# Kernel tuning notes

Measured on AMD Instinct MI355X. Metric: run time of the kernel, lower is better.

The kernel has to match this reference:

```python
import jax, jax.numpy as jnp
import numpy as np

H = 256          # hidden_size
HH, WW = 4, 4
CONV = HH * WW * H   # 4096, conv_out_size
N = 16           # n_subtasks
S = 32           # subtask_size
B = 256          # batch
T = 128          # timesteps
TOT = N + S + H + S + 1 + 1  # 338, RecurrentState width


def setup_inputs() -> dict:
    key = jax.random.key(0)
    ks = jax.random.split(key, 12)
    w = lambda k, shape: (jax.random.normal(k, shape) * 0.02).astype(jnp.float32)
    obs = jax.random.normal(ks[0], (T, B, CONV), jnp.float32)
    task = jax.random.normal(ks[1], (B, N, S), jnp.float32)
    hx0 = jnp.zeros((B, TOT), jnp.float32).at[:, :N].set(1.0 / N)  # uniform pointer init
    return dict(
        obs=obs, task=task, hx0=hx0,
        W_ih=w(ks[2], (3 * H, H)), W_hh=w(ks[3], (3 * H, H)),
        b_ih=jnp.zeros((3 * H,), jnp.float32), b_hh=jnp.zeros((3 * H,), jnp.float32),
        W_f=w(ks[4], (H, CONV + 2 * S + 1)), b_f=jnp.zeros((H,), jnp.float32),
        W_u=w(ks[5], (1, 2 * H)), b_u=jnp.zeros((1,), jnp.float32),
        W_s=w(ks[6], (3, H)), b_s=jnp.zeros((3,), jnp.float32),
        W_pi=w(ks[7], (N, H + S)), b_pi=jnp.zeros((N,), jnp.float32),
        W_beta=w(ks[8], (2, CONV + S)), b_beta=jnp.zeros((2,), jnp.float32),
    )


def reference(obs, task, hx0, W_ih, W_hh, b_ih, b_hh, W_f, b_f, W_u, b_u,
              W_s, b_s, W_pi, b_pi, W_beta, b_beta):
    M = task  # [B, N, S] subtask memory
    p0 = hx0[:, :N]
    r0 = hx0[:, N:N + S]
    h0 = hx0[:, N + S:N + S + H]
    g0 = hx0[:, N + S + H:N + S + H + S]
    b0 = hx0[:, N + S + H + S:N + S + H + S + 1]
    keys = jax.random.split(jax.random.key(42), T * 2).reshape(T, 2)

    def gru(x, h):  # torch.nn.GRUCell math
        gi = x @ W_ih.T + b_ih
        gh = h @ W_hh.T + b_hh
        ir, iz, inn = jnp.split(gi, 3, axis=-1)
        hr, hz, hn = jnp.split(gh, 3, axis=-1)
        rr = jax.nn.sigmoid(ir + hr)
        z = jax.nn.sigmoid(iz + hz)
        n = jnp.tanh(inn + rr * hn)
        return (1.0 - z) * n + z * h

    def step(carry, xs):
        p, r, h, b = carry[0], carry[1], carry[2], carry[4]
        g = carry[3]
        x, kk = xs
        # s = f(cat(x, r, g, b))
        s = jnp.concatenate([x, r, g, b], axis=-1) @ W_f.T + b_f
        # update gate c = sigmoid(phi_update(cat(s, h)))
        c = jax.nn.sigmoid(jnp.concatenate([s, h], axis=-1) @ W_u.T + b_u)  # [B,1]
        h_new = gru(s, h)
        # pointer shift: l = softmax(phi_shift(h_old)); p = conv1d(p, l) (same-pad, k=3)
        l = jax.nn.softmax(h @ W_s.T + b_s, axis=1)  # [B,3]
        pp = jnp.pad(p, ((0, 0), (1, 1)))
        p_new = l[:, 0:1] * pp[:, :N] + l[:, 1:2] * pp[:, 1:N + 1] + l[:, 2:3] * pp[:, 2:N + 2]
        # memory read r = p @ M
        r_new = jnp.einsum('bn,bns->bs', p_new, M)
        p = c * p_new + (1.0 - c) * p
        r = c * r_new + (1.0 - c) * r
        h = c * h_new + (1.0 - c) * h
        # sample g ~ Cat(pi_theta(h, r)); g embedding = selected memory row
        logits_g = jnp.concatenate([h, r], axis=-1) @ W_pi.T + b_pi  # [B,N]
        g_idx = jax.random.categorical(kk[0], logits_g)  # [B] int
        lp_g = jnp.take_along_axis(jax.nn.log_softmax(logits_g, axis=-1), g_idx[:, None], axis=1)  # [B,1]
        g_vec = jnp.take_along_axis(M, g_idx[:, None, None], axis=1)[:, 0, :]  # [B,S]
        g = c * g_vec + (1.0 - c) * g
        # sample b ~ Cat(beta(x, g))
        logits_b = jnp.concatenate([x, g], axis=-1) @ W_beta.T + b_beta  # [B,2]
        b_idx = jax.random.categorical(kk[1], logits_b)
        lp_b = jnp.take_along_axis(jax.nn.log_softmax(logits_b, axis=-1), b_idx[:, None], axis=1)
        b = b_idx[:, None].astype(jnp.float32)
        log_prob = lp_g + lp_b
        out = jnp.concatenate([p, r, h, g, b, log_prob], axis=-1)  # [B, TOT]
        return (p, r, h, g, b), out

    _, outs = jax.lax.scan(step, (p0, r0, h0, g0, b0), (obs, keys))
    return outs  # [T, B, TOT]
```

## Files before the change

### kernel.cpp

```cpp
#include <hip/hip_runtime.h>


#define RNG_PARTITIONABLE 1

#define T_STEPS 128
#define B_ROWS  256
#define TOT     338
#define CONV    4096
#define LDWF    4161
#define LDWB    4128

__device__ __forceinline__ void tf2x32(unsigned k0, unsigned k1, unsigned c0, unsigned c1,
                                       unsigned &o0, unsigned &o1) {
  const unsigned ks2 = k0 ^ k1 ^ 0x1BD11BDAu;
  unsigned x0 = c0 + k0;
  unsigned x1 = c1 + k1;
#define TFR(r) { x0 += x1; x1 = (x1 << (r)) | (x1 >> (32 - (r))); x1 ^= x0; }
  TFR(13) TFR(15) TFR(26) TFR(6)
  x0 += k1; x1 += ks2 + 1u;
  TFR(17) TFR(29) TFR(16) TFR(24)
  x0 += ks2; x1 += k0 + 2u;
  TFR(13) TFR(15) TFR(26) TFR(6)
  x0 += k0; x1 += k1 + 3u;
  TFR(17) TFR(29) TFR(16) TFR(24)
  x0 += k1; x1 += ks2 + 4u;
  TFR(13) TFR(15) TFR(26) TFR(6)
  x0 += ks2; x1 += k0 + 5u;
#undef TFR
  o0 = x0; o1 = x1;
}

__device__ __forceinline__ void rng_key(unsigned j, unsigned &k0, unsigned &k1) {
#if RNG_PARTITIONABLE
  tf2x32(0u, 42u, 0u, j, k0, k1);
#else
  unsigned w[2];
  for (int q = 0; q < 2; ++q) {
    unsigned i = 2u*j + (unsigned)q, a, b;
    if (i < 256u) { tf2x32(0u, 42u, i, 256u + i, a, b); w[q] = a; }
    else          { tf2x32(0u, 42u, i - 256u, i, a, b); w[q] = b; }
  }
  k0 = w[0]; k1 = w[1];
#endif
}

__device__ __forceinline__ unsigned rng_bits(unsigned k0, unsigned k1, unsigned idx, unsigned total) {
#if RNG_PARTITIONABLE
  unsigned o0, o1;
  tf2x32(k0, k1, 0u, idx, o0, o1);
  return o0 ^ o1;
#else
  unsigned half = total >> 1, o0, o1;
  if (idx < half) { tf2x32(k0, k1, idx, half + idx, o0, o1); return o0; }
  else            { tf2x32(k0, k1, idx - half, idx, o0, o1); return o1; }
#endif
}

__device__ __forceinline__ float gumbel_from_bits(unsigned bits) {
  float u0 = __uint_as_float(0x3f800000u | (bits >> 9)) - 1.0f;
  float u  = fmaxf(u0, 1.17549435e-38f);
  return -logf(-logf(u));
}

__global__ __launch_bounds__(256) void rng_k(float* __restrict__ ggum, float* __restrict__ bgum) {
  unsigned tid = blockIdx.x * 256u + threadIdx.x;
  const unsigned NG = T_STEPS * B_ROWS * 16;
  const unsigned NB = T_STEPS * B_ROWS * 2;
  if (tid < NG) {
    unsigned t = tid / (B_ROWS * 16);
    unsigned i = tid % (B_ROWS * 16);
    unsigned k0, k1; rng_key(2u * t, k0, k1);
    ggum[tid] = gumbel_from_bits(rng_bits(k0, k1, i, B_ROWS * 16));
  } else if (tid < NG + NB) {
    unsigned q = tid - NG;
    unsigned t = q / (B_ROWS * 2);
    unsigned i = q % (B_ROWS * 2);
    unsigned k0, k1; rng_key(2u * t + 1u, k0, k1);
    bgum[q] = gumbel_from_bits(rng_bits(k0, k1, i, B_ROWS * 2));
  }
}

__global__ __launch_bounds__(256) void prep2_k(const float* __restrict__ W_ih,
                                               const float* __restrict__ W_hh,
                                               float2* __restrict__ WT2) {
  int col = blockIdx.x;
  int k = threadIdx.x;
  WT2[(size_t)k * 768 + col] =
      make_float2(W_ih[(size_t)col * 256 + k], W_hh[(size_t)col * 256 + k]);
}

__device__ __forceinline__ float waveRed(float v) {
  v += __shfl_down(v, 32, 64);
  v += __shfl_down(v, 16, 64);
  v += __shfl_down(v, 8, 64);
  v += __shfl_down(v, 4, 64);
  v += __shfl_down(v, 2, 64);
  v += __shfl_down(v, 1, 64);
  return v;
}

__global__ __launch_bounds__(256) void bx_k(const float* __restrict__ obs,
                                            const float* __restrict__ W_beta,
                                            const float* __restrict__ b_beta,
                                            float* __restrict__ bxv) {
  int m = blockIdx.x, tid = threadIdx.x;
  const float* row = obs + (size_t)m * CONV;
  float p0 = 0.f, p1 = 0.f;
  for (int i = tid; i < CONV; i += 256) {
    float o = row[i];
    p0 = fmaf(o, W_beta[i], p0);
    p1 = fmaf(o, W_beta[LDWB + i], p1);
  }
  p0 = waveRed(p0); p1 = waveRed(p1);
  __shared__ float sc[2][4];
  int w = tid >> 6;
  if ((tid & 63) == 0) { sc[0][w] = p0; sc[1][w] = p1; }
  __syncthreads();
  if (tid == 0) bxv[(size_t)m * 2 + 0] = sc[0][0] + sc[0][1] + sc[0][2] + sc[0][3] + b_beta[0];
  if (tid == 1) bxv[(size_t)m * 2 + 1] = sc[1][0] + sc[1][1] + sc[1][2] + sc[1][3] + b_beta[1];
}

struct __attribute__((packed, aligned(4))) F4 { float x, y, z, w; };

__global__ __launch_bounds__(256) void gemm1_k(const float* __restrict__ A,
                                               const float* __restrict__ W,
                                               const float* __restrict__ bias,
                                               float* __restrict__ C1) {
  __shared__ __align__(16) float As[32][68];
  __shared__ __align__(16) float Bs[32][68];
  int bid = blockIdx.x;
  int mt = bid & 511, nt = bid >> 9;
  int m0 = mt * 64, n0 = nt * 64;
  int tid = threadIdx.x;
  int tm = tid & 15, tn = tid >> 4;
  int lr = tid >> 2;
  int lc = (tid & 3) * 8;
  float acc[4][4] = {};
  for (int k0 = 0; k0 < CONV; k0 += 32) {
    F4 a0 = *(const F4*)(A + (size_t)(m0 + lr) * CONV + k0 + lc);
    F4 a1 = *(const F4*)(A + (size_t)(m0 + lr) * CONV + k0 + lc + 4);
    F4 b0 = *(const F4*)(W + (size_t)(n0 + lr) * LDWF + k0 + lc);
    F4 b1 = *(const F4*)(W + (size_t)(n0 + lr) * LDWF + k0 + lc + 4);
    __syncthreads();
    As[lc + 0][lr] = a0.x; As[lc + 1][lr] = a0.y; As[lc + 2][lr] = a0.z; As[lc + 3][lr] = a0.w;
    As[lc + 4][lr] = a1.x; As[lc + 5][lr] = a1.y; As[lc + 6][lr] = a1.z; As[lc + 7][lr] = a1.w;
    Bs[lc + 0][lr] = b0.x; Bs[lc + 1][lr] = b0.y; Bs[lc + 2][lr] = b0.z; Bs[lc + 3][lr] = b0.w;
    Bs[lc + 4][lr] = b1.x; Bs[lc + 5][lr] = b1.y; Bs[lc + 6][lr] = b1.z; Bs[lc + 7][lr] = b1.w;
    __syncthreads();
#pragma unroll
    for (int kk = 0; kk < 32; ++kk) {
      const float4 av = *(const float4*)&As[kk][tm * 4];
      const float4 bv = *(const float4*)&Bs[kk][tn * 4];
      acc[0][0] = fmaf(av.x, bv.x, acc[0][0]); acc[0][1] = fmaf(av.x, bv.y, acc[0][1]);
      acc[0][2] = fmaf(av.x, bv.z, acc[0][2]); acc[0][3] = fmaf(av.x, bv.w, acc[0][3]);
      acc[1][0] = fmaf(av.y, bv.x, acc[1][0]); acc[1][1] = fmaf(av.y, bv.y, acc[1][1]);
      acc[1][2] = fmaf(av.y, bv.z, acc[1][2]); acc[1][3] = fmaf(av.y, bv.w, acc[1][3]);
      acc[2][0] = fmaf(av.z, bv.x, acc[2][0]); acc[2][1] = fmaf(av.z, bv.y, acc[2][1]);
      acc[2][2] = fmaf(av.z, bv.z, acc[2][2]); acc[2][3] = fmaf(av.z, bv.w, acc[2][3]);
      acc[3][0] = fmaf(av.w, bv.x, acc[3][0]); acc[3][1] = fmaf(av.w, bv.y, acc[3][1]);
      acc[3][2] = fmaf(av.w, bv.z, acc[3][2]); acc[3][3] = fmaf(av.w, bv.w, acc[3][3]);
    }
  }
  const int mrow = m0 + tm * 4;
  const int ncol = n0 + tn * 4;
  float4 bv4 = *(const float4*)(bias + ncol);
#pragma unroll
  for (int i = 0; i < 4; ++i) {
    float4 v;
    v.x = acc[i][0] + bv4.x; v.y = acc[i][1] + bv4.y;
    v.z = acc[i][2] + bv4.z; v.w = acc[i][3] + bv4.w;
    *(float4*)(C1 + (size_t)(mrow + i) * 256 + ncol) = v;
  }
}

__global__ __launch_bounds__(768, 1) void seq_k(
    const float* __restrict__ hx0, const float* __restrict__ task,
    const float* __restrict__ W_f, const float* __restrict__ WT2,
    const float* __restrict__ b_ih, const float* __restrict__ b_hh,
    const float* __restrict__ W_u, const float* __restrict__ b_u,
    const float* __restrict__ W_s, const float* __restrict__ b_s,
    const float* __restrict__ W_pi, const float* __restrict__ b_pi,
    const float* __restrict__ W_beta, const float* __restrict__ C1,
    const float* __restrict__ bxv, const float* __restrict__ ggum,
    const float* __restrict__ bgum, float* __restrict__ out) {
  const int b = blockIdx.x;
  const int tid = threadIdx.x;
  const int o = tid & 255;
  const int part = tid >> 8;
  const float2* __restrict__ WT2v = (const float2*)WT2;

  __shared__ float wf_sh[65 * 256];
  __shared__ float wpi_sh[288 * 16];
  __shared__ float2 shb[256];
  __shared__ float2 gsum[2][256];
  __shared__ float M_sh[512];
  __shared__ float p_sh[16], pn_sh[16], r_sh[32], g_sh[32];
  __shared__ float red4[4][4];
  __shared__ float red16[4][16];
  __shared__ float logit_sh[16];
  __shared__ float l_sh[3];
  __shared__ float c_sh, b_sh;
  __shared__ int gidx_sh;
  __shared__ float misc_sh[3];
  __shared__ float gg_sh[16], bg_sh[2], bx_sh[2];
  __shared__ float wb_sh[2][32], bpi_sh[16];

  for (int i = tid; i < 65 * 256; i += 768) {
    int oo = i / 65, j = i % 65;
    wf_sh[i] = W_f[(size_t)oo * LDWF + CONV + j];
  }
  for (int i = tid; i < 288 * 16; i += 768) wpi_sh[i] = W_pi[i];
  if (part == 0) shb[o] = make_float2(0.f, hx0[b * TOT + 48 + o]);
  if (tid < 16) p_sh[tid] = hx0[b * TOT + tid];
  if (tid < 32) {
    r_sh[tid] = hx0[b * TOT + 16 + tid];
    g_sh[tid] = hx0[b * TOT + 304 + tid];
    wb_sh[0][tid] = W_beta[CONV + tid];
    wb_sh[1][tid] = W_beta[LDWB + CONV + tid];
  }
  if (tid >= 32 && tid < 48) bpi_sh[tid - 32] = b_pi[tid - 32];
  if (tid == 0) b_sh = hx0[b * TOT + 336];
  if (tid < 512) M_sh[tid] = task[(size_t)b * 512 + tid];

  const float bih_r = b_ih[o], bih_z = b_ih[256 + o], bih_n = b_ih[512 + o];
  const float bhh_r = b_hh[o], bhh_z = b_hh[256 + o], bhh_n = b_hh[512 + o];
  const float wu_s = W_u[o], wu_h = W_u[256 + o];
  const float ws0 = W_s[o], ws1 = W_s[256 + o], ws2 = W_s[512 + o];
  const float bu0 = b_u[0], bs0 = b_s[0], bs1 = b_s[1], bs2 = b_s[2];
  __syncthreads();

  float c1v = (part == 0) ? C1[(size_t)b * 256 + o] : 0.f;
  float sacc = 0.f, hold = 0.f;

  for (int t = 0; t < T_STEPS; ++t) {
    if (part == 0) {
      hold = shb[o].y;
      sacc = c1v;
      const float* wfr = wf_sh + o * 65;
#pragma unroll
      for (int j = 0; j < 32; ++j) sacc = fmaf(r_sh[j], wfr[j], sacc);
#pragma unroll
      for (int j = 0; j < 32; ++j) sacc = fmaf(g_sh[j], wfr[32 + j], sacc);
      sacc = fmaf(b_sh, wfr[64], sacc);
      shb[o].x = sacc;
    }
    __syncthreads();

    if (part == 0) {
      int tn2 = (t + 1 < T_STEPS) ? t + 1 : t;
      c1v = C1[((size_t)tn2 * 256 + b) * 256 + o];
    } else if (tid < 272) {
      gg_sh[tid - 256] = ggum[((size_t)t * 256 + b) * 16 + (tid - 256)];
    } else if (tid < 274) {
      bg_sh[tid - 272] = bgum[((size_t)t * 256 + b) * 2 + (tid - 272)];
    } else if (tid < 276) {
      bx_sh[tid - 274] = bxv[((size_t)t * 256 + b) * 2 + (tid - 274)];
    }

    float ai = 0.f, ah = 0.f;
#pragma unroll 8
    for (int k = 0; k < 256; ++k) {
      float2 w = WT2v[(size_t)k * 768 + tid];
      float2 sh2 = shb[k];
      ai = fmaf(sh2.x, w.x, ai);
      ah = fmaf(sh2.y, w.y, ah);
    }
    if (part == 0) {
      float pc = fmaf(wu_s, sacc, wu_h * hold);
      float q0 = ws0 * hold, q1 = ws1 * hold, q2 = ws2 * hold;
      pc = waveRed(pc); q0 = waveRed(q0); q1 = waveRed(q1); q2 = waveRed(q2);
      int w4 = tid >> 6;
      if ((tid & 63) == 0) { red4[w4][0] = pc; red4[w4][1] = q0; red4[w4][2] = q1; red4[w4][3] = q2; }
    } else {
      gsum[part - 1][o] = make_float2(ai, ah);
    }
    __syncthreads();
    if (tid == 0) {
      float cs = red4[0][0] + red4[1][0] + red4[2][0] + red4[3][0] + bu0;
      c_sh = 1.0f / (1.0f + expf(-cs));
      float x0 = red4[0][1] + red4[1][1] + red4[2][1] + red4[3][1] + bs0;
      float x1 = red4[0][2] + red4[1][2] + red4[2][2] + red4[3][2] + bs1;
      float x2 = red4[0][3] + red4[1][3] + red4[2][3] + red4[3][3] + bs2;
      float m = fmaxf(x0, fmaxf(x1, x2));
      float e0 = expf(x0 - m), e1 = expf(x1 - m), e2 = expf(x2 - m);
      float es = e0 + e1 + e2;
      l_sh[0] = e0 / es; l_sh[1] = e1 / es; l_sh[2] = e2 / es;
    }
    __syncthreads();
    const float c = c_sh, omc = 1.0f - c;
    float hg = 0.f;
    if (part == 0) {
      float2 gz = gsum[0][o];
      float2 gn = gsum[1][o];
      float rr = 1.0f / (1.0f + expf(-(ai + bih_r + ah + bhh_r)));
      float zz = 1.0f / (1.0f + expf(-(gz.x + bih_z + gz.y + bhh_z)));
      float nn = tanhf(gn.x + bih_n + rr * (gn.y + bhh_n));
      float hnew = (1.0f - zz) * nn + zz * hold;
      hg = c * hnew + omc * hold;
      shb[o].y = hg;
    }
    if (tid < 16) {
      float pm1 = (tid > 0) ? p_sh[tid - 1] : 0.f;
      float pp1 = (tid < 15) ? p_sh[tid + 1] : 0.f;
      pn_sh[tid] = l_sh[0] * pm1 + l_sh[1] * p_sh[tid] + l_sh[2] * pp1;
    }
    __syncthreads();
    float rv = 0.f;
    if (tid < 32) {
      float acc = 0.f;
#pragma unroll
      for (int n2 = 0; n2 < 16; ++n2) acc = fmaf(pn_sh[n2], M_sh[n2 * 32 + tid], acc);
      rv = c * acc + omc * r_sh[tid];
      r_sh[tid] = rv;
    }
    if (tid < 16) p_sh[tid] = c * pn_sh[tid] + omc * p_sh[tid];
    if (part == 0) {
      float pv[16];
#pragma unroll
      for (int o2 = 0; o2 < 16; ++o2) pv[o2] = hg * wpi_sh[o2 * 288 + tid];
      if (tid < 32) {
#pragma unroll
        for (int o2 = 0; o2 < 16; ++o2) pv[o2] = fmaf(rv, wpi_sh[o2 * 288 + 256 + tid], pv[o2]);
      }
#pragma unroll
      for (int o2 = 0; o2 < 16; ++o2) pv[o2] = waveRed(pv[o2]);
      int w4 = tid >> 6;
      if ((tid & 63) == 0) {
#pragma unroll
        for (int o2 = 0; o2 < 16; ++o2) red16[w4][o2] = pv[o2];
      }
    }
    __syncthreads();
    if (tid < 16)
      logit_sh[tid] = red16[0][tid] + red16[1][tid] + red16[2][tid] + red16[3][tid] + bpi_sh[tid];
    __syncthreads();
    if (tid == 0) {
      float best = -3.402823466e+38f; int gidx = 0;
      for (int n2 = 0; n2 < 16; ++n2) {
        float v = logit_sh[n2] + gg_sh[n2];
        if (v > best) { best = v; gidx = n2; }
      }
      float mx = logit_sh[0];
      for (int n2 = 1; n2 < 16; ++n2) mx = fmaxf(mx, logit_sh[n2]);
      float se = 0.f;
      for (int n2 = 0; n2 < 16; ++n2) se += expf(logit_sh[n2] - mx);
      misc_sh[0] = logit_sh[gidx] - mx - logf(se);
      gidx_sh = gidx;
    }
    __syncthreads();
    if (tid < 32) g_sh[tid] = c * M_sh[gidx_sh * 32 + tid] + omc * g_sh[tid];
    __syncthreads();
    if (tid == 0) {
      float lb0 = bx_sh[0], lb1 = bx_sh[1];
      for (int s2 = 0; s2 < 32; ++s2) {
        float gv = g_sh[s2];
        lb0 = fmaf(gv, wb_sh[0][s2], lb0);
        lb1 = fmaf(gv, wb_sh[1][s2], lb1);
      }
      int bidx = ((lb1 + bg_sh[1]) > (lb0 + bg_sh[0])) ? 1 : 0;
      float mb = fmaxf(lb0, lb1);
      float seb = expf(lb0 - mb) + expf(lb1 - mb);
      float lpb = (bidx ? lb1 : lb0) - mb - logf(seb);
      misc_sh[1] = (float)bidx;
      misc_sh[2] = misc_sh[0] + lpb;
      b_sh = (float)bidx;
    }
    __syncthreads();
    if (tid < TOT) {
      size_t base = ((size_t)t * 256 + b) * TOT;
      float v;
      if (tid < 16) v = p_sh[tid];
      else if (tid < 48) v = r_sh[tid - 16];
      else if (tid < 304) v = shb[tid - 48].y;
      else if (tid < 336) v = g_sh[tid - 304];
      else if (tid == 336) v = misc_sh[1];
      else v = misc_sh[2];
      out[base + tid] = v;
    }
    __syncthreads();
  }
}

extern "C" void kernel_launch(void* const* d_in, const int* in_sizes, int n_in,
                              void* d_out, int out_size, void* d_ws, size_t ws_size,
                              hipStream_t stream) {
  const float* obs    = (const float*)d_in[0];
  const float* task   = (const float*)d_in[1];
  const float* hx0    = (const float*)d_in[2];
  const float* W_ih   = (const float*)d_in[3];
  const float* W_hh   = (const float*)d_in[4];
  const float* b_ih   = (const float*)d_in[5];
  const float* b_hh   = (const float*)d_in[6];
  const float* W_f    = (const float*)d_in[7];
  const float* b_f    = (const float*)d_in[8];
  const float* W_u    = (const float*)d_in[9];
  const float* b_u    = (const float*)d_in[10];
  const float* W_s    = (const float*)d_in[11];
  const float* b_s    = (const float*)d_in[12];
  const float* W_pi   = (const float*)d_in[13];
  const float* b_pi   = (const float*)d_in[14];
  const float* W_beta = (const float*)d_in[15];
  const float* b_beta = (const float*)d_in[16];

  char* ws = (char*)d_ws;
  size_t off = 0;
  auto take = [&](size_t bytes) {
    size_t r = off;
    off += (bytes + 255) & ~(size_t)255;
    return r;
  };
  size_t off_WT2  = take((size_t)768 * 256 * 8);
  size_t off_ggum = take((size_t)T_STEPS * B_ROWS * 16 * 4);
  size_t off_bgum = take((size_t)T_STEPS * B_ROWS * 2 * 4);
  size_t off_bx   = take((size_t)T_STEPS * B_ROWS * 2 * 4);
  size_t off_C1   = take((size_t)T_STEPS * B_ROWS * 256 * 4);
  if (off > ws_size) return;

  float* WT2  = (float*)(ws + off_WT2);
  float* ggum = (float*)(ws + off_ggum);
  float* bgum = (float*)(ws + off_bgum);
  float* bxv  = (float*)(ws + off_bx);
  float* C1   = (float*)(ws + off_C1);

  hipLaunchKernelGGL(prep2_k, dim3(768), dim3(256), 0, stream, W_ih, W_hh, (float2*)WT2);
  hipLaunchKernelGGL(rng_k, dim3(2304), dim3(256), 0, stream, ggum, bgum);
  hipLaunchKernelGGL(gemm1_k, dim3(2048), dim3(256), 0, stream, obs, W_f, b_f, C1);
  hipLaunchKernelGGL(bx_k, dim3(32768), dim3(256), 0, stream, obs, W_beta, b_beta, bxv);
  hipLaunchKernelGGL(seq_k, dim3(256), dim3(768), 0, stream,
                     hx0, task, W_f, WT2, b_ih, b_hh, W_u, b_u, W_s, b_s, W_pi, b_pi,
                     W_beta, C1, bxv, ggum, bgum, (float*)d_out);
}
```

Before: 4.590 ms.

## Process four batch rows per sequential block and use packed FMA in GEMM

The sequential recurrent kernel now handles four batch rows per block (64 blocks of 1024 threads instead of 256 of 768). Each load of the W_ih/W_hh weights from global memory is reused across four rows, using packed two-wide FMAs on interleaved hidden-state vectors. This cuts the weight traffic per step roughly fourfold but uses only 64 workgroups, leaving most compute units idle, and adds more per-row shared state. The obs GEMM inner loop is also rewritten with two-wide vector FMAs in the hope of emitting packed FMA instructions.

```diff
diff --git a/kernel.cpp b/kernel.cpp
--- a/kernel.cpp
+++ b/kernel.cpp
@@ -9,6 +9,8 @@
 #define CONV    4096
 #define LDWF    4161
 #define LDWB    4128
+
+typedef float v2f __attribute__((ext_vector_type(2)));
 
 __device__ __forceinline__ void tf2x32(unsigned k0, unsigned k1, unsigned c0, unsigned c1,
                                        unsigned &o0, unsigned &o1) {
@@ -135,7 +137,9 @@
   int tm = tid & 15, tn = tid >> 4;
   int lr = tid >> 2;
   int lc = (tid & 3) * 8;
-  float acc[4][4] = {};
+  v2f acc[4][2];
+#pragma unroll
+  for (int i = 0; i < 4; ++i) { acc[i][0] = (v2f){0.f, 0.f}; acc[i][1] = (v2f){0.f, 0.f}; }
   for (int k0 = 0; k0 < CONV; k0 += 32) {
     F4 a0 = *(const F4*)(A + (size_t)(m0 + lr) * CONV + k0 + lc);
     F4 a1 = *(const F4*)(A + (size_t)(m0 + lr) * CONV + k0 + lc + 4);
@@ -151,14 +155,15 @@
     for (int kk = 0; kk < 32; ++kk) {
       const float4 av = *(const float4*)&As[kk][tm * 4];
       const float4 bv = *(const float4*)&Bs[kk][tn * 4];
-      acc[0][0] = fmaf(av.x, bv.x, acc[0][0]); acc[0][1] = fmaf(av.x, bv.y, acc[0][1]);
-      acc[0][2] = fmaf(av.x, bv.z, acc[0][2]); acc[0][3] = fmaf(av.x, bv.w, acc[0][3]);
-      acc[1][0] = fmaf(av.y, bv.x, acc[1][0]); acc[1][1] = fmaf(av.y, bv.y, acc[1][1]);
-      acc[1][2] = fmaf(av.y, bv.z, acc[1][2]); acc[1][3] = fmaf(av.y, bv.w, acc[1][3]);
-      acc[2][0] = fmaf(av.z, bv.x, acc[2][0]); acc[2][1] = fmaf(av.z, bv.y, acc[2][1]);
-      acc[2][2] = fmaf(av.z, bv.z, acc[2][2]); acc[2][3] = fmaf(av.z, bv.w, acc[2][3]);
-      acc[3][0] = fmaf(av.w, bv.x, acc[3][0]); acc[3][1] = fmaf(av.w, bv.y, acc[3][1]);
-      acc[3][2] = fmaf(av.w, bv.z, acc[3][2]); acc[3][3] = fmaf(av.w, bv.w, acc[3][3]);
+      const v2f bl = (v2f){bv.x, bv.y};
+      const v2f bh = (v2f){bv.z, bv.w};
+      const float aa[4] = {av.x, av.y, av.z, av.w};
+#pragma unroll
+      for (int i = 0; i < 4; ++i) {
+        v2f ax = (v2f){aa[i], aa[i]};
+        acc[i][0] = __builtin_elementwise_fma(ax, bl, acc[i][0]);
+        acc[i][1] = __builtin_elementwise_fma(ax, bh, acc[i][1]);
+      }
     }
   }
   const int mrow = m0 + tm * 4;
@@ -167,13 +172,13 @@
 #pragma unroll
   for (int i = 0; i < 4; ++i) {
     float4 v;
-    v.x = acc[i][0] + bv4.x; v.y = acc[i][1] + bv4.y;
-    v.z = acc[i][2] + bv4.z; v.w = acc[i][3] + bv4.w;
+    v.x = acc[i][0].x + bv4.x; v.y = acc[i][0].y + bv4.y;
+    v.z = acc[i][1].x + bv4.z; v.w = acc[i][1].y + bv4.w;
     *(float4*)(C1 + (size_t)(mrow + i) * 256 + ncol) = v;
   }
 }
 
-__global__ __launch_bounds__(768, 1) void seq_k(
+__global__ __launch_bounds__(1024, 1) void seq_k(
     const float* __restrict__ hx0, const float* __restrict__ task,
     const float* __restrict__ W_f, const float* __restrict__ WT2,
     const float* __restrict__ b_ih, const float* __restrict__ b_hh,
@@ -183,44 +188,51 @@
     const float* __restrict__ W_beta, const float* __restrict__ C1,
     const float* __restrict__ bxv, const float* __restrict__ ggum,
     const float* __restrict__ bgum, float* __restrict__ out) {
-  const int b = blockIdx.x;
+  const int b4 = blockIdx.x;
   const int tid = threadIdx.x;
+  const int r = tid >> 8;
   const int o = tid & 255;
-  const int part = tid >> 8;
+  const int brow = b4 * 4 + r;
   const float2* __restrict__ WT2v = (const float2*)WT2;
 
   __shared__ float wf_sh[65 * 256];
   __shared__ float wpi_sh[288 * 16];
-  __shared__ float2 shb[256];
-  __shared__ float2 gsum[2][256];
-  __shared__ float M_sh[512];
-  __shared__ float p_sh[16], pn_sh[16], r_sh[32], g_sh[32];
-  __shared__ float red4[4][4];
-  __shared__ float red16[4][16];
-  __shared__ float logit_sh[16];
-  __shared__ float l_sh[3];
-  __shared__ float c_sh, b_sh;
-  __shared__ int gidx_sh;
-  __shared__ float misc_sh[3];
-  __shared__ float gg_sh[16], bg_sh[2], bx_sh[2];
+  __shared__ float4 sh01[256];
+  __shared__ float4 sh23[256];
+  __shared__ float gpub[24][256];
+  __shared__ float M_sh[4][512];
+  __shared__ float p_sh[4][16], pn_sh[4][16], r_sh[4][32], g_sh[4][32];
+  __shared__ float red4[4][4][4];
+  __shared__ float red16[4][4][16];
+  __shared__ float logit_sh[4][16];
+  __shared__ float l_sh[4][3];
+  __shared__ float c_sh[4], b_sh[4];
+  __shared__ int gidx_sh[4];
+  __shared__ float misc_sh[4][3];
+  __shared__ float gg_sh[4][16], bg_sh[4][2], bx_sh[4][2];
   __shared__ float wb_sh[2][32], bpi_sh[16];
 
-  for (int i = tid; i < 65 * 256; i += 768) {
+  for (int i = tid; i < 65 * 256; i += 1024) {
     int oo = i / 65, j = i % 65;
     wf_sh[i] = W_f[(size_t)oo * LDWF + CONV + j];
   }
-  for (int i = tid; i < 288 * 16; i += 768) wpi_sh[i] = W_pi[i];
-  if (part == 0) shb[o] = make_float2(0.f, hx0[b * TOT + 48 + o]);
-  if (tid < 16) p_sh[tid] = hx0[b * TOT + tid];
+  for (int i = tid; i < 288 * 16; i += 1024) wpi_sh[i] = W_pi[i];
+  float* shp = (r < 2) ? (float*)&sh01[o] : (float*)&sh23[o];
+  const int rc = r & 1;
+  shp[2 + rc] = hx0[brow * TOT + 48 + o];
+  if (o < 16) p_sh[r][o] = hx0[brow * TOT + o];
+  if (o < 32) {
+    r_sh[r][o] = hx0[brow * TOT + 16 + o];
+    g_sh[r][o] = hx0[brow * TOT + 304 + o];
+  }
+  if (o == 0) b_sh[r] = hx0[brow * TOT + 336];
+  M_sh[r][o] = task[(size_t)brow * 512 + o];
+  M_sh[r][256 + o] = task[(size_t)brow * 512 + 256 + o];
   if (tid < 32) {
-    r_sh[tid] = hx0[b * TOT + 16 + tid];
-    g_sh[tid] = hx0[b * TOT + 304 + tid];
     wb_sh[0][tid] = W_beta[CONV + tid];
     wb_sh[1][tid] = W_beta[LDWB + CONV + tid];
   }
   if (tid >= 32 && tid < 48) bpi_sh[tid - 32] = b_pi[tid - 32];
-  if (tid == 0) b_sh = hx0[b * TOT + 336];
-  if (tid < 512) M_sh[tid] = task[(size_t)b * 512 + tid];
 
   const float bih_r = b_ih[o], bih_z = b_ih[256 + o], bih_n = b_ih[512 + o];
   const float bhh_r = b_hh[o], bhh_z = b_hh[256 + o], bhh_n = b_hh[512 + o];
@@ -229,153 +241,172 @@
   const float bu0 = b_u[0], bs0 = b_s[0], bs1 = b_s[1], bs2 = b_s[2];
   __syncthreads();
 
-  float c1v = (part == 0) ? C1[(size_t)b * 256 + o] : 0.f;
-  float sacc = 0.f, hold = 0.f;
+  float c1v = C1[(size_t)brow * 256 + o];
 
   for (int t = 0; t < T_STEPS; ++t) {
-    if (part == 0) {
-      hold = shb[o].y;
-      sacc = c1v;
+    const float hold = shp[2 + rc];
+    float sacc = c1v;
+    {
       const float* wfr = wf_sh + o * 65;
 #pragma unroll
-      for (int j = 0; j < 32; ++j) sacc = fmaf(r_sh[j], wfr[j], sacc);
-#pragma unroll
-      for (int j = 0; j < 32; ++j) sacc = fmaf(g_sh[j], wfr[32 + j], sacc);
-      sacc = fmaf(b_sh, wfr[64], sacc);
-      shb[o].x = sacc;
-    }
-    __syncthreads();
-
-    if (part == 0) {
+      for (int j = 0; j < 32; ++j) sacc = fmaf(r_sh[r][j], wfr[j], sacc);
+#pragma unroll
+      for (int j = 0; j < 32; ++j) sacc = fmaf(g_sh[r][j], wfr[32 + j], sacc);
+      sacc = fmaf(b_sh[r], wfr[64], sacc);
+      shp[rc] = sacc;
+    }
+    __syncthreads();
+
+    {
       int tn2 = (t + 1 < T_STEPS) ? t + 1 : t;
-      c1v = C1[((size_t)tn2 * 256 + b) * 256 + o];
-    } else if (tid < 272) {
-      gg_sh[tid - 256] = ggum[((size_t)t * 256 + b) * 16 + (tid - 256)];
-    } else if (tid < 274) {
-      bg_sh[tid - 272] = bgum[((size_t)t * 256 + b) * 2 + (tid - 272)];
-    } else if (tid < 276) {
-      bx_sh[tid - 274] = bxv[((size_t)t * 256 + b) * 2 + (tid - 274)];
-    }
-
-    float ai = 0.f, ah = 0.f;
+      c1v = C1[((size_t)tn2 * 256 + brow) * 256 + o];
+    }
+
+    if (tid < 768) {
+      v2f ai01 = (v2f){0.f, 0.f}, ah01 = (v2f){0.f, 0.f};
+      v2f ai23 = (v2f){0.f, 0.f}, ah23 = (v2f){0.f, 0.f};
 #pragma unroll 8
-    for (int k = 0; k < 256; ++k) {
-      float2 w = WT2v[(size_t)k * 768 + tid];
-      float2 sh2 = shb[k];
-      ai = fmaf(sh2.x, w.x, ai);
-      ah = fmaf(sh2.y, w.y, ah);
-    }
-    if (part == 0) {
+      for (int k = 0; k < 256; ++k) {
+        float2 w = WT2v[(size_t)k * 768 + tid];
+        float4 v01 = sh01[k];
+        float4 v23 = sh23[k];
+        v2f wx = (v2f){w.x, w.x};
+        v2f wy = (v2f){w.y, w.y};
+        ai01 = __builtin_elementwise_fma((v2f){v01.x, v01.y}, wx, ai01);
+        ah01 = __builtin_elementwise_fma((v2f){v01.z, v01.w}, wy, ah01);
+        ai23 = __builtin_elementwise_fma((v2f){v23.x, v23.y}, wx, ai23);
+        ah23 = __builtin_elementwise_fma((v2f){v23.z, v23.w}, wy, ah23);
+      }
+      const int part = tid >> 8, oo = tid & 255;
+      gpub[0 + part][oo]  = ai01.x;  gpub[3 + part][oo]  = ah01.x;
+      gpub[6 + part][oo]  = ai01.y;  gpub[9 + part][oo]  = ah01.y;
+      gpub[12 + part][oo] = ai23.x;  gpub[15 + part][oo] = ah23.x;
+      gpub[18 + part][oo] = ai23.y;  gpub[21 + part][oo] = ah23.y;
+    } else if (tid < 832) {
+      int q = tid - 768, rr = q >> 4;
+      gg_sh[rr][q & 15] = ggum[((size_t)t * 256 + b4 * 4 + rr) * 16 + (q & 15)];
+    } else if (tid < 840) {
+      int q = tid - 832, rr = q >> 1;
+      bg_sh[rr][q & 1] = bgum[((size_t)t * 256 + b4 * 4 + rr) * 2 + (q & 1)];
+    } else if (tid < 848) {
+      int q = tid - 840, rr = q >> 1;
+      bx_sh[rr][q & 1] = bxv[((size_t)t * 256 + b4 * 4 + rr) * 2 + (q & 1)];
+    }
+    {
       float pc = fmaf(wu_s, sacc, wu_h * hold);
       float q0 = ws0 * hold, q1 = ws1 * hold, q2 = ws2 * hold;
       pc = waveRed(pc); q0 = waveRed(q0); q1 = waveRed(q1); q2 = waveRed(q2);
-      int w4 = tid >> 6;
-      if ((tid & 63) == 0) { red4[w4][0] = pc; red4[w4][1] = q0; red4[w4][2] = q1; red4[w4][3] = q2; }
-    } else {
-      gsum[part - 1][o] = make_float2(ai, ah);
-    }
-    __syncthreads();
-    if (tid == 0) {
-      float cs = red4[0][0] + red4[1][0] + red4[2][0] + red4[3][0] + bu0;
-      c_sh = 1.0f / (1.0f + expf(-cs));
-      float x0 = red4[0][1] + red4[1][1] + red4[2][1] + red4[3][1] + bs0;
-      float x1 = red4[0][2] + red4[1][2] + red4[2][2] + red4[3][2] + bs1;
-      float x2 = red4[0][3] + red4[1][3] + red4[2][3] + red4[3][3] + bs2;
+      int w4 = (tid >> 6) & 3;
+      if ((tid & 63) == 0) { red4[r][w4][0] = pc; red4[r][w4][1] = q0; red4[r][w4][2] = q1; red4[r][w4][3] = q2; }
+    }
+    __syncthreads();
+    if (o == 0) {
+      float cs = red4[r][0][0] + red4[r][1][0] + red4[r][2][0] + red4[r][3][0] + bu0;
+      c_sh[r] = 1.0f / (1.0f + expf(-cs));
+      float x0 = red4[r][0][1] + red4[r][1][1] + red4[r][2][1] + red4[r][3][1] + bs0;
+      float x1 = red4[r][0][2] + red4[r][1][2] + red4[r][2][2] + red4[r][3][2] + bs1;
+      float x2 = red4[r][0][3] + red4[r][1][3] + red4[r][2][3] + red4[r][3][3] + bs2;
       float m = fmaxf(x0, fmaxf(x1, x2));
       float e0 = expf(x0 - m), e1 = expf(x1 - m), e2 = expf(x2 - m);
       float es = e0 + e1 + e2;
-      l_sh[0] = e0 / es; l_sh[1] = e1 / es; l_sh[2] = e2 / es;
-    }
-    __syncthreads();
-    const float c = c_sh, omc = 1.0f - c;
-    float hg = 0.f;
-    if (part == 0) {
-      float2 gz = gsum[0][o];
-      float2 gn = gsum[1][o];
-      float rr = 1.0f / (1.0f + expf(-(ai + bih_r + ah + bhh_r)));
-      float zz = 1.0f / (1.0f + expf(-(gz.x + bih_z + gz.y + bhh_z)));
-      float nn = tanhf(gn.x + bih_n + rr * (gn.y + bhh_n));
+      l_sh[r][0] = e0 / es; l_sh[r][1] = e1 / es; l_sh[r][2] = e2 / es;
+    }
+    __syncthreads();
+    const float c = c_sh[r], omc = 1.0f - c;
+
+    float hg;
+    {
+      float air = gpub[r * 6 + 0][o], aiz = gpub[r * 6 + 1][o], ain = gpub[r * 6 + 2][o];
+      float ahr = gpub[r * 6 + 3][o], ahz = gpub[r * 6 + 4][o], ahn = gpub[r * 6 + 5][o];
+      float rr_ = 1.0f / (1.0f + expf(-(air + bih_r + ahr + bhh_r)));
+      float zz = 1.0f / (1.0f + expf(-(aiz + bih_z + ahz + bhh_z)));
+      float nn = tanhf(ain + bih_n + rr_ * (ahn + bhh_n));
       float hnew = (1.0f - zz) * nn + zz * hold;
       hg = c * hnew + omc * hold;
-      shb[o].y = hg;
-    }
-    if (tid < 16) {
-      float pm1 = (tid > 0) ? p_sh[tid - 1] : 0.f;
-      float pp1 = (tid < 15) ? p_sh[tid + 1] : 0.f;
-      pn_sh[tid] = l_sh[0] * pm1 + l_sh[1] * p_sh[tid] + l_sh[2] * pp1;
+      shp[2 + rc] = hg;
+    }
+    if (o < 16) {
+      float pm1 = (o > 0) ? p_sh[r][o - 1] : 0.f;
+      float pp1 = (o < 15) ? p_sh[r][o + 1] : 0.f;
+      pn_sh[r][o] = l_sh[r][0] * pm1 + l_sh[r][1] * p_sh[r][o] + l_sh[r][2] * pp1;
     }
     __syncthreads();
     float rv = 0.f;
-    if (tid < 32) {
+    if (o < 32) {
       float acc = 0.f;
 #pragma unroll
-      for (int n2 = 0; n2 < 16; ++n2) acc = fmaf(pn_sh[n2], M_sh[n2 * 32 + tid], acc);
-      rv = c * acc + omc * r_sh[tid];
-      r_sh[tid] = rv;
-    }
-    if (tid < 16) p_sh[tid] = c * pn_sh[tid] + omc * p_sh[tid];
-    if (part == 0) {
+      for (int n2 = 0; n2 < 16; ++n2) acc = fmaf(pn_sh[r][n2], M_sh[r][n2 * 32 + o], acc);
+      rv = c * acc + omc * r_sh[r][o];
+      r_sh[r][o] = rv;
+    }
+    if (o < 16) p_sh[r][o] = c * pn_sh[r][o] + omc * p_sh[r][o];
+    {
       float pv[16];
 #pragma unroll
-      for (int o2 = 0; o2 < 16; ++o2) pv[o2] = hg * wpi_sh[o2 * 288 + tid];
-      if (tid < 32) {
-#pragma unroll
-        for (int o2 = 0; o2 < 16; ++o2) pv[o2] = fmaf(rv, wpi_sh[o2 * 288 + 256 + tid], pv[o2]);
+      for (int o2 = 0; o2 < 16; ++o2) pv[o2] = hg * wpi_sh[o2 * 288 + o];
+      if (o < 32) {
+#pragma unroll
+        for (int o2 = 0; o2 < 16; ++o2) pv[o2] = fmaf(rv, wpi_sh[o2 * 288 + 256 + o], pv[o2]);
       }
 #pragma unroll
       for (int o2 = 0; o2 < 16; ++o2) pv[o2] = waveRed(pv[o2]);
-      int w4 = tid >> 6;
+      int w4 = (tid >> 6) & 3;
       if ((tid & 63) == 0) {
 #pragma unroll
-        for (int o2 = 0; o2 < 16; ++o2) red16[w4][o2] = pv[o2];
-      }
-    }
-    __syncthreads();
-    if (tid < 16)
-      logit_sh[tid] = red16[0][tid] + red16[1][tid] + red16[2][tid] + red16[3][tid] + bpi_sh[tid];
-    __syncthreads();
-    if (tid == 0) {
+        for (int o2 = 0; o2 < 16; ++o2) red16[r][w4][o2] = pv[o2];
+      }
+    }
+    __syncthreads();
+    if (o < 16)
+      logit_sh[r][o] = red16[r][0][o] + red16[r][1][o] + red16[r][2][o] + red16[r][3][o] + bpi_sh[o];
+    __syncthreads();
+    if (o == 0) {
       float best = -3.402823466e+38f; int gidx = 0;
       for (int n2 = 0; n2 < 16; ++n2) {
-        float v = logit_sh[n2] + gg_sh[n2];
+        float v = logit_sh[r][n2] + gg_sh[r][n2];
         if (v > best) { best = v; gidx = n2; }
       }
-      float mx = logit_sh[0];
-      for (int n2 = 1; n2 < 16; ++n2) mx = fmaxf(mx, logit_sh[n2]);
+      float mx = logit_sh[r][0];
+      for (int n2 = 1; n2 < 16; ++n2) mx = fmaxf(mx, logit_sh[r][n2]);
       float se = 0.f;
-      for (int n2 = 0; n2 < 16; ++n2) se += expf(logit_sh[n2] - mx);
-      misc_sh[0] = logit_sh[gidx] - mx - logf(se);
-      gidx_sh = gidx;
-    }
-    __syncthreads();
-    if (tid < 32) g_sh[tid] = c * M_sh[gidx_sh * 32 + tid] + omc * g_sh[tid];
-    __syncthreads();
-    if (tid == 0) {
-      float lb0 = bx_sh[0], lb1 = bx_sh[1];
+      for (int n2 = 0; n2 < 16; ++n2) se += expf(logit_sh[r][n2] - mx);
+      misc_sh[r][0] = logit_sh[r][gidx] - mx - logf(se);
+      gidx_sh[r] = gidx;
+    }
+    __syncthreads();
+    if (o < 32) g_sh[r][o] = c * M_sh[r][gidx_sh[r] * 32 + o] + omc * g_sh[r][o];
+    __syncthreads();
+    if (o == 0) {
+      float lb0 = bx_sh[r][0], lb1 = bx_sh[r][1];
       for (int s2 = 0; s2 < 32; ++s2) {
-        float gv = g_sh[s2];
+        float gv = g_sh[r][s2];
         lb0 = fmaf(gv, wb_sh[0][s2], lb0);
         lb1 = fmaf(gv, wb_sh[1][s2], lb1);
       }
-      int bidx = ((lb1 + bg_sh[1]) > (lb0 + bg_sh[0])) ? 1 : 0;
+      int bidx = ((lb1 + bg_sh[r][1]) > (lb0 + bg_sh[r][0])) ? 1 : 0;
       float mb = fmaxf(lb0, lb1);
       float seb = expf(lb0 - mb) + expf(lb1 - mb);
       float lpb = (bidx ? lb1 : lb0) - mb - logf(seb);
-      misc_sh[1] = (float)bidx;
-      misc_sh[2] = misc_sh[0] + lpb;
-      b_sh = (float)bidx;
-    }
-    __syncthreads();
-    if (tid < TOT) {
-      size_t base = ((size_t)t * 256 + b) * TOT;
+      misc_sh[r][1] = (float)bidx;
+      misc_sh[r][2] = misc_sh[r][0] + lpb;
+      b_sh[r] = (float)bidx;
+    }
+    __syncthreads();
+    for (int q = tid; q < 4 * TOT; q += 1024) {
+      int rr2 = q / TOT;
+      int j = q - rr2 * TOT;
       float v;
-      if (tid < 16) v = p_sh[tid];
-      else if (tid < 48) v = r_sh[tid - 16];
-      else if (tid < 304) v = shb[tid - 48].y;
-      else if (tid < 336) v = g_sh[tid - 304];
-      else if (tid == 336) v = misc_sh[1];
-      else v = misc_sh[2];
-      out[base + tid] = v;
+      if (j < 16) v = p_sh[rr2][j];
+      else if (j < 48) v = r_sh[rr2][j - 16];
+      else if (j < 304) {
+        int hh = j - 48;
+        const float* hp = (rr2 < 2) ? (const float*)&sh01[hh] : (const float*)&sh23[hh];
+        v = hp[2 + (rr2 & 1)];
+      }
+      else if (j < 336) v = g_sh[rr2][j - 304];
+      else if (j == 336) v = misc_sh[rr2][1];
+      else v = misc_sh[rr2][2];
+      out[((size_t)t * 256 + b4 * 4 + rr2) * TOT + j] = v;
     }
     __syncthreads();
   }
@@ -426,7 +457,7 @@
   hipLaunchKernelGGL(rng_k, dim3(2304), dim3(256), 0, stream, ggum, bgum);
   hipLaunchKernelGGL(gemm1_k, dim3(2048), dim3(256), 0, stream, obs, W_f, b_f, C1);
   hipLaunchKernelGGL(bx_k, dim3(32768), dim3(256), 0, stream, obs, W_beta, b_beta, bxv);
-  hipLaunchKernelGGL(seq_k, dim3(256), dim3(768), 0, stream,
+  hipLaunchKernelGGL(seq_k, dim3(64), dim3(1024), 0, stream,
                      hx0, task, W_f, WT2, b_ih, b_hh, W_u, b_u, W_s, b_s, W_pi, b_pi,
                      W_beta, C1, bxv, ggum, bgum, (float*)d_out);
 }
```

After: 6.858 ms. 49.4% more time.
